# Kernel optimization log

Measured on AMD Instinct MI355X. Metric: run time of the kernel, lower is better.

Reference implementation:

```python
import jax, jax.numpy as jnp
import numpy as np

N = 50000   # query points
N2 = 50000  # key/value points
C = 128     # n_channels
G = 8       # n_groups
S = 16      # n_samples
CS = C // G # n_share_channels
EPS = 1e-5


def setup_inputs() -> dict:
    key = jax.random.key(0)
    ks = jax.random.split(key, 16)
    std = 0.02
    return {
        "p": jax.random.normal(ks[0], (N, 3), jnp.float32),
        "x": jax.random.normal(ks[1], (N, C), jnp.float32),
        "p2": jax.random.normal(ks[2], (N2, 3), jnp.float32),
        "x2": jax.random.normal(ks[3], (N2, C), jnp.float32),
        "idx": jax.random.randint(ks[4], (N, S), 0, N2, jnp.int32),
        "Wq": jax.random.normal(ks[5], (C, C), jnp.float32) * std,
        "bq": jnp.zeros((C,), jnp.float32),
        "Wk": jax.random.normal(ks[6], (C, C), jnp.float32) * std,
        "bk": jnp.zeros((C,), jnp.float32),
        "Wv": jax.random.normal(ks[7], (C, C), jnp.float32) * std,
        "bv": jnp.zeros((C,), jnp.float32),
        # linear_p: Conv1d(3,3,1) -> BN(3) -> ReLU -> Conv1d(3, 2G, 1)
        "W1": jax.random.normal(ks[8], (3, 3), jnp.float32) * 0.5,
        "b1": jnp.zeros((3,), jnp.float32),
        "bn_gamma": jnp.ones((3,), jnp.float32),
        "bn_beta": jnp.zeros((3,), jnp.float32),
        "bn_mean": jnp.zeros((3,), jnp.float32),
        "bn_var": jnp.ones((3,), jnp.float32),
        "W2": jax.random.normal(ks[9], (2 * G, 3), jnp.float32) * 0.5,
        "b2": jnp.zeros((2 * G,), jnp.float32),
    }


def reference(p, x, p2, x2, idx,
              Wq, bq, Wk, bk, Wv, bv,
              W1, b1, bn_gamma, bn_beta, bn_mean, bn_var, W2, b2):
    n = x.shape[0]
    # Q/K/V projections
    x_q = x @ Wq.T + bq                       # (n, C)
    x_k = (x2 @ Wk.T + bk)[idx]               # (n, S, C)  KNN gather
    x_v = (x2 @ Wv.T + bv)[idx]               # (n, S, C)
    # relative positions
    p_r = p2[idx] - p[:, None, :]             # (n, S, 3)
    # linear_p (pointwise convs == per-neighbor MLP over the 3 coord channels)
    h = p_r @ W1.T + b1
    h = (h - bn_mean) * jax.lax.rsqrt(bn_var + EPS) * bn_gamma + bn_beta
    h = jax.nn.relu(h)
    pe = h @ W2.T + b2                        # (n, S, 2G)
    p_rq, p_rk = jnp.split(pe, 2, axis=-1)    # each (n, S, G)
    # grouped attention
    k4 = x_k.reshape(n, S, G, CS) + p_rk[..., None]
    q4 = x_q.reshape(n, 1, G, CS) + p_rq[..., None]
    logits = jnp.sum(k4 * q4, axis=-1) / np.float32(np.sqrt(CS))  # (n, S, G)
    w = jax.nn.softmax(logits, axis=1)        # softmax over neighbors
    out = jnp.einsum('nsgc,nsg->ngc', x_v.reshape(n, S, G, CS), w)
    return out.reshape(n, C)
```

## Files before the change

### kernel.cpp

```cpp
#include <hip/hip_runtime.h>
#include <hip/hip_bf16.h>

#define NQ   50000
#define NKV  50000
#define CC   128
#define GG   8
#define SS   16
#define CSH  16

typedef short    bf16x8 __attribute__((ext_vector_type(8)));
typedef float    f32x4  __attribute__((ext_vector_type(4)));
typedef unsigned u32x4  __attribute__((ext_vector_type(4)));
typedef unsigned u32x2  __attribute__((ext_vector_type(2)));
typedef int      i32x4  __attribute__((ext_vector_type(4)));

__device__ __forceinline__ float bf_lo(unsigned u){ union{unsigned x; float f;} v; v.x = u << 16;        return v.f; }
__device__ __forceinline__ float bf_hi(unsigned u){ union{unsigned x; float f;} v; v.x = u & 0xffff0000u; return v.f; }
__device__ __forceinline__ unsigned short f2bfu(float f){
    __hip_bfloat16 h = __float2bfloat16(f);
    return *reinterpret_cast<unsigned short*>(&h);
}
__device__ __forceinline__ short f2bfs(float f){
    __hip_bfloat16 h = __float2bfloat16(f);
    return *reinterpret_cast<short*>(&h);
}

__device__ __forceinline__ void load16bf(const __hip_bfloat16* ptr, float* o){
    const u32x4* p4 = reinterpret_cast<const u32x4*>(ptr);
    u32x4 a = p4[0]; u32x4 b = p4[1];
    o[0]=bf_lo(a[0]);  o[1]=bf_hi(a[0]);  o[2]=bf_lo(a[1]);  o[3]=bf_hi(a[1]);
    o[4]=bf_lo(a[2]);  o[5]=bf_hi(a[2]);  o[6]=bf_lo(a[3]);  o[7]=bf_hi(a[3]);
    o[8]=bf_lo(b[0]);  o[9]=bf_hi(b[0]);  o[10]=bf_lo(b[1]); o[11]=bf_hi(b[1]);
    o[12]=bf_lo(b[2]); o[13]=bf_hi(b[2]); o[14]=bf_lo(b[3]); o[15]=bf_hi(b[3]);
}

__device__ __forceinline__ bf16x8 cvt8(const float* p){
    const f32x4* q = reinterpret_cast<const f32x4*>(p);
    f32x4 u = q[0], v = q[1];
    bf16x8 r;
    r[0]=f2bfs(u[0]); r[1]=f2bfs(u[1]); r[2]=f2bfs(u[2]); r[3]=f2bfs(u[3]);
    r[4]=f2bfs(v[0]); r[5]=f2bfs(v[1]); r[6]=f2bfs(v[2]); r[7]=f2bfs(v[3]);
    return r;
}

__global__ __launch_bounds__(256) void qkv_gemm(
    const float* __restrict__ x,
    const float* __restrict__ x2,
    const float* __restrict__ Wq, const float* __restrict__ Wk,
    const float* __restrict__ Wv,
    const float* __restrict__ bq, const float* __restrict__ bk,
    const float* __restrict__ bv,
    __hip_bfloat16* __restrict__ Qf,
    __hip_bfloat16* __restrict__ KVf)
{
    __shared__ short lds16[16384];

    const int tid  = threadIdx.x;
    const int wave = tid >> 6;
    const int lane = tid & 63;
    const int r    = lane & 15;
    const int kq   = lane >> 4;
    const int base = blockIdx.x * 128 + wave * 32;
    const int proj = blockIdx.y;

    const float* src  = (proj == 0) ? x  : x2;
    const float* W    = (proj == 0) ? Wq : (proj == 1 ? Wk : Wv);
    const float* bias = (proj == 0) ? bq : (proj == 1 ? bk : bv);
    short* dstb   = (proj == 0) ? (short*)Qf : (short*)KVf;
    const int dstride = (proj == 0) ? CC : 2 * CC;
    const int hoff    = (proj == 2) ? CC : 0;

    bf16x8 bfrag[2][4];
    #pragma unroll
    for (int mt = 0; mt < 2; ++mt) {
        int row = base + mt * 16 + r;
        if (row >= NQ) row = NQ - 1;
        const float* xr = src + (size_t)row * CC + kq * 8;
        #pragma unroll
        for (int kb = 0; kb < 4; ++kb)
            bfrag[mt][kb] = cvt8(xr + kb * 32);
    }

    #pragma unroll
    for (int i = 0; i < 8; ++i) {
        const int o   = i * 2048 + tid * 8;
        const bf16x8 v = cvt8(W + o);
        const int row = o >> 7, col = o & 127;
        const int lchunk = (((row >> 4) * 4 + (col >> 5)) << 6)
                         + (((col >> 3) & 3) << 4) + (row & 15);
        *reinterpret_cast<bf16x8*>(&lds16[lchunk * 8]) = v;
    }
    __syncthreads();

    #pragma unroll
    for (int t = 0; t < 8; ++t) {
        bf16x8 af[4];
        #pragma unroll
        for (int kb = 0; kb < 4; ++kb)
            af[kb] = *reinterpret_cast<const bf16x8*>(
                &lds16[(((t * 4 + kb) << 6) + lane) * 8]);

        f32x4 acc0 = {0.f,0.f,0.f,0.f}, acc1 = {0.f,0.f,0.f,0.f};
        #pragma unroll
        for (int kb = 0; kb < 4; ++kb) {
            acc0 = __builtin_amdgcn_mfma_f32_16x16x32_bf16(af[kb], bfrag[0][kb], acc0, 0, 0, 0);
            acc1 = __builtin_amdgcn_mfma_f32_16x16x32_bf16(af[kb], bfrag[1][kb], acc1, 0, 0, 0);
        }

        const f32x4 bi = *reinterpret_cast<const f32x4*>(bias + t * 16 + kq * 4);
        #pragma unroll
        for (int mt = 0; mt < 2; ++mt) {
            const int row = base + mt * 16 + r;
            if (row < NQ) {
                const f32x4 a = mt ? acc1 : acc0;
                u32x2 pk;
                pk[0] = (unsigned)f2bfu(a[0] + bi[0]) | ((unsigned)f2bfu(a[1] + bi[1]) << 16);
                pk[1] = (unsigned)f2bfu(a[2] + bi[2]) | ((unsigned)f2bfu(a[3] + bi[3]) << 16);
                *reinterpret_cast<u32x2*>(
                    dstb + (size_t)row * dstride + hoff + t * 16 + kq * 4) = pk;
            }
        }
    }
}

__global__ __launch_bounds__(256) void attn_kernel(
    const float* __restrict__ p,
    const float* __restrict__ p2,
    const int*   __restrict__ idx,
    const float* __restrict__ W1,
    const float* __restrict__ b1,
    const float* __restrict__ bn_gamma,
    const float* __restrict__ bn_beta,
    const float* __restrict__ bn_mean,
    const float* __restrict__ bn_var,
    const float* __restrict__ W2,
    const float* __restrict__ b2,
    const __hip_bfloat16* __restrict__ Qf,
    const __hip_bfloat16* __restrict__ KVf,
    float* __restrict__ out)
{
    const int tid = blockIdx.x * 256 + threadIdx.x;
    if (tid >= NQ * GG) return;
    const int n = tid >> 3;
    const int g = tid & 7;

    float fw1[3][3], fb1[3];
    #pragma unroll
    for (int j = 0; j < 3; ++j) {
        const float sc = bn_gamma[j] * rsqrtf(bn_var[j] + 1e-5f);
        #pragma unroll
        for (int k = 0; k < 3; ++k) fw1[j][k] = W1[j*3 + k] * sc;
        fb1[j] = (b1[j] - bn_mean[j]) * sc + bn_beta[j];
    }
    const float w2q0 = W2[g*3+0],     w2q1 = W2[g*3+1],     w2q2 = W2[g*3+2];
    const float w2k0 = W2[(g+8)*3+0], w2k1 = W2[(g+8)*3+1], w2k2 = W2[(g+8)*3+2];
    const float b2q = b2[g], b2k = b2[g+8];

    const float px = p[(size_t)n*3+0];
    const float py = p[(size_t)n*3+1];
    const float pz = p[(size_t)n*3+2];

    int nbr[SS];
    {
        const i32x4* ip = reinterpret_cast<const i32x4*>(idx + (size_t)n * SS);
        i32x4 i0 = ip[0], i1 = ip[1], i2 = ip[2], i3 = ip[3];
        nbr[0]=i0[0]; nbr[1]=i0[1]; nbr[2]=i0[2]; nbr[3]=i0[3];
        nbr[4]=i1[0]; nbr[5]=i1[1]; nbr[6]=i1[2]; nbr[7]=i1[3];
        nbr[8]=i2[0]; nbr[9]=i2[1]; nbr[10]=i2[2]; nbr[11]=i2[3];
        nbr[12]=i3[0]; nbr[13]=i3[1]; nbr[14]=i3[2]; nbr[15]=i3[3];
    }

    float q[CSH];
    load16bf(Qf + (size_t)n * CC + g * CSH, q);
    float sumq = 0.f;
    #pragma unroll
    for (int c = 0; c < CSH; ++c) sumq += q[c];

    float d[SS];
    #pragma unroll
    for (int s = 0; s < SS; ++s) {
        const int i = nbr[s];
        float kk[CSH];
        load16bf(KVf + (size_t)i * (2 * CC) + g * CSH, kk);

        const float rx = p2[(size_t)i*3+0] - px;
        const float ry = p2[(size_t)i*3+1] - py;
        const float rz = p2[(size_t)i*3+2] - pz;
        const float h0 = fmaxf(fw1[0][0]*rx + fw1[0][1]*ry + fw1[0][2]*rz + fb1[0], 0.f);
        const float h1 = fmaxf(fw1[1][0]*rx + fw1[1][1]*ry + fw1[1][2]*rz + fb1[1], 0.f);
        const float h2 = fmaxf(fw1[2][0]*rx + fw1[2][1]*ry + fw1[2][2]*rz + fb1[2], 0.f);
        const float prq = w2q0*h0 + w2q1*h1 + w2q2*h2 + b2q;
        const float prk = w2k0*h0 + w2k1*h1 + w2k2*h2 + b2k;

        float dot = 0.f, sumk = 0.f;
        #pragma unroll
        for (int c = 0; c < CSH; ++c) { dot += kk[c]*q[c]; sumk += kk[c]; }
        d[s] = (dot + prq*sumk + prk*sumq + 16.f*prk*prq) * 0.25f;
    }

    float m = d[0];
    #pragma unroll
    for (int s = 1; s < SS; ++s) m = fmaxf(m, d[s]);
    float w[SS], sum = 0.f;
    #pragma unroll
    for (int s = 0; s < SS; ++s) { w[s] = __expf(d[s] - m); sum += w[s]; }
    const float inv = 1.f / sum;
    #pragma unroll
    for (int s = 0; s < SS; ++s) w[s] *= inv;

    float acc[CSH];
    #pragma unroll
    for (int c = 0; c < CSH; ++c) acc[c] = 0.f;
    #pragma unroll
    for (int s = 0; s < SS; ++s) {
        const int i = nbr[s];
        float vv[CSH];
        load16bf(KVf + (size_t)i * (2 * CC) + CC + g * CSH, vv);
        #pragma unroll
        for (int c = 0; c < CSH; ++c) acc[c] += w[s] * vv[c];
    }

    f32x4* op = reinterpret_cast<f32x4*>(out + (size_t)n * CC + g * CSH);
    f32x4 o0 = {acc[0],  acc[1],  acc[2],  acc[3]};
    f32x4 o1 = {acc[4],  acc[5],  acc[6],  acc[7]};
    f32x4 o2 = {acc[8],  acc[9],  acc[10], acc[11]};
    f32x4 o3 = {acc[12], acc[13], acc[14], acc[15]};
    op[0] = o0; op[1] = o1; op[2] = o2; op[3] = o3;
}

extern "C" void kernel_launch(void* const* d_in, const int* in_sizes, int n_in,
                              void* d_out, int out_size, void* d_ws, size_t ws_size,
                              hipStream_t stream) {
    const float* p   = (const float*)d_in[0];
    const float* x   = (const float*)d_in[1];
    const float* p2  = (const float*)d_in[2];
    const float* x2  = (const float*)d_in[3];
    const int*   idx = (const int*)d_in[4];
    const float* Wq  = (const float*)d_in[5];
    const float* bq  = (const float*)d_in[6];
    const float* Wk  = (const float*)d_in[7];
    const float* bk  = (const float*)d_in[8];
    const float* Wv  = (const float*)d_in[9];
    const float* bv  = (const float*)d_in[10];
    const float* W1  = (const float*)d_in[11];
    const float* b1  = (const float*)d_in[12];
    const float* bng = (const float*)d_in[13];
    const float* bnb = (const float*)d_in[14];
    const float* bnm = (const float*)d_in[15];
    const float* bnv = (const float*)d_in[16];
    const float* W2  = (const float*)d_in[17];
    const float* b2  = (const float*)d_in[18];
    float* out = (float*)d_out;

    __hip_bfloat16* Qf  = (__hip_bfloat16*)d_ws;
    __hip_bfloat16* KVf = Qf + (size_t)NQ * CC;

    qkv_gemm<<<dim3(391, 3), 256, 0, stream>>>(
        x, x2, Wq, Wk, Wv, bq, bk, bv, Qf, KVf);

    const int nthreads = NQ * GG;
    attn_kernel<<<(nthreads + 255) / 256, 256, 0, stream>>>(
        p, p2, idx, W1, b1, bng, bnb, bnm, bnv, W2, b2, Qf, KVf, out);
}
```

Measured before the change: 227.5 us.

## Split neighbors across thread pairs with online softmax and shuffle merge

Each (query, group) is now handled by two threads, each covering 8 of the 16 neighbors. The separate score and value passes become one online-softmax pass, and the two partial states are combined with lane shuffles. This doubles thread count and halves per-thread register arrays, meant to raise memory-level parallelism and occupancy for the gather-bound kernel. The cost is extra exp work for the running-max correction and shuffle traffic. The bounds check is dropped because 3125 blocks of 256 threads exactly cover 50000×16.

New measurement: 208.6 us. -8.3%, faster.

```diff
diff --git a/kernel.cpp b/kernel.cpp
--- a/kernel.cpp
+++ b/kernel.cpp
@@ -140,9 +140,9 @@
     float* __restrict__ out)
 {
     const int tid = blockIdx.x * 256 + threadIdx.x;
-    if (tid >= NQ * GG) return;
-    const int n = tid >> 3;
-    const int g = tid & 7;
+    const int n = tid >> 4;
+    const int g = (tid >> 1) & 7;
+    const int h = tid & 1;
 
     float fw1[3][3], fb1[3];
     #pragma unroll
@@ -160,14 +160,12 @@
     const float py = p[(size_t)n*3+1];
     const float pz = p[(size_t)n*3+2];
 
-    int nbr[SS];
+    int nbr[8];
     {
-        const i32x4* ip = reinterpret_cast<const i32x4*>(idx + (size_t)n * SS);
-        i32x4 i0 = ip[0], i1 = ip[1], i2 = ip[2], i3 = ip[3];
+        const i32x4* ip = reinterpret_cast<const i32x4*>(idx + (size_t)n * SS + h * 8);
+        i32x4 i0 = ip[0], i1 = ip[1];
         nbr[0]=i0[0]; nbr[1]=i0[1]; nbr[2]=i0[2]; nbr[3]=i0[3];
         nbr[4]=i1[0]; nbr[5]=i1[1]; nbr[6]=i1[2]; nbr[7]=i1[3];
-        nbr[8]=i2[0]; nbr[9]=i2[1]; nbr[10]=i2[2]; nbr[11]=i2[3];
-        nbr[12]=i3[0]; nbr[13]=i3[1]; nbr[14]=i3[2]; nbr[15]=i3[3];
     }
 
     float q[CSH];
@@ -176,12 +174,20 @@
     #pragma unroll
     for (int c = 0; c < CSH; ++c) sumq += q[c];
 
-    float d[SS];
-    #pragma unroll
-    for (int s = 0; s < SS; ++s) {
+    float acc[CSH];
+    #pragma unroll
+    for (int c = 0; c < CSH; ++c) acc[c] = 0.f;
+    float sum = 0.f;
+    float m = -3.0e38f;
+
+    #pragma unroll 4
+    for (int s = 0; s < 8; ++s) {
         const int i = nbr[s];
-        float kk[CSH];
-        load16bf(KVf + (size_t)i * (2 * CC) + g * CSH, kk);
+        const __hip_bfloat16* kv = KVf + (size_t)i * (2 * CC) + g * CSH;
+
+        float kk[CSH], vv[CSH];
+        load16bf(kv, kk);
+        load16bf(kv + CC, vv);
 
         const float rx = p2[(size_t)i*3+0] - px;
         const float ry = p2[(size_t)i*3+1] - py;
@@ -195,37 +201,38 @@
         float dot = 0.f, sumk = 0.f;
         #pragma unroll
         for (int c = 0; c < CSH; ++c) { dot += kk[c]*q[c]; sumk += kk[c]; }
-        d[s] = (dot + prq*sumk + prk*sumq + 16.f*prk*prq) * 0.25f;
-    }
-
-    float m = d[0];
-    #pragma unroll
-    for (int s = 1; s < SS; ++s) m = fmaxf(m, d[s]);
-    float w[SS], sum = 0.f;
-    #pragma unroll
-    for (int s = 0; s < SS; ++s) { w[s] = __expf(d[s] - m); sum += w[s]; }
-    const float inv = 1.f / sum;
-    #pragma unroll
-    for (int s = 0; s < SS; ++s) w[s] *= inv;
-
-    float acc[CSH];
-    #pragma unroll
-    for (int c = 0; c < CSH; ++c) acc[c] = 0.f;
-    #pragma unroll
-    for (int s = 0; s < SS; ++s) {
-        const int i = nbr[s];
-        float vv[CSH];
-        load16bf(KVf + (size_t)i * (2 * CC) + CC + g * CSH, vv);
-        #pragma unroll
-        for (int c = 0; c < CSH; ++c) acc[c] += w[s] * vv[c];
-    }
-
-    f32x4* op = reinterpret_cast<f32x4*>(out + (size_t)n * CC + g * CSH);
-    f32x4 o0 = {acc[0],  acc[1],  acc[2],  acc[3]};
-    f32x4 o1 = {acc[4],  acc[5],  acc[6],  acc[7]};
-    f32x4 o2 = {acc[8],  acc[9],  acc[10], acc[11]};
-    f32x4 o3 = {acc[12], acc[13], acc[14], acc[15]};
-    op[0] = o0; op[1] = o1; op[2] = o2; op[3] = o3;
+        const float d = (dot + prq*sumk + prk*sumq + 16.f*prk*prq) * 0.25f;
+
+        const float mnew = fmaxf(m, d);
+        const float corr = __expf(m - mnew);
+        const float w    = __expf(d - mnew);
+        sum = sum * corr + w;
+        #pragma unroll
+        for (int c = 0; c < CSH; ++c) acc[c] = acc[c] * corr + w * vv[c];
+        m = mnew;
+    }
+
+    const float mo = __shfl_xor(m, 1);
+    const float M  = fmaxf(m, mo);
+    const float cs = __expf(m  - M);
+    const float co = __expf(mo - M);
+    const float so = __shfl_xor(sum, 1);
+    const float inv = 1.f / (sum * cs + so * co);
+    const float mycs = cs * inv, pco = co * inv;
+
+    float o[8];
+    #pragma unroll
+    for (int j = 0; j < 8; ++j) {
+        const float send = h ? acc[j] : acc[j + 8];
+        const float recv = __shfl_xor(send, 1);
+        const float own  = h ? acc[j + 8] : acc[j];
+        o[j] = own * mycs + recv * pco;
+    }
+
+    f32x4* op = reinterpret_cast<f32x4*>(out + (size_t)n * CC + g * CSH + h * 8);
+    f32x4 o0 = {o[0], o[1], o[2], o[3]};
+    f32x4 o1 = {o[4], o[5], o[6], o[7]};
+    op[0] = o0; op[1] = o1;
 }
 
 extern "C" void kernel_launch(void* const* d_in, const int* in_sizes, int n_in,
@@ -258,7 +265,6 @@
     qkv_gemm<<<dim3(391, 3), 256, 0, stream>>>(
         x, x2, Wq, Wk, Wv, bq, bk, bv, Qf, KVf);
 
-    const int nthreads = NQ * GG;
-    attn_kernel<<<(nthreads + 255) / 256, 256, 0, stream>>>(
+    attn_kernel<<<3125, 256, 0, stream>>>(
         p, p2, idx, W1, b1, bng, bnb, bnm, bnv, W2, b2, Qf, KVf, out);
 }
```
